# Performance work log

Hardware: AMD Instinct MI355X
Metric: run time of the kernel (lower is better)

## Reference

```python
import jax, jax.numpy as jnp
import numpy as np

N_GAUSSIANS = 512
N_PIXELS = 262144  # 512x512 image


def setup_inputs() -> dict:
    key = jax.random.key(0)
    k1, k2, k3, k4, k5 = jax.random.split(key, 5)
    x = jax.random.uniform(k1, (N_PIXELS, 2), dtype=jnp.float32)
    alphas = (1.0 / N_GAUSSIANS) ** 0.5 * jax.random.uniform(k2, (N_GAUSSIANS, 1), dtype=jnp.float32)
    means = jax.random.uniform(k3, (N_GAUSSIANS, 2), dtype=jnp.float32)
    rotations = jnp.pi * jax.random.uniform(k4, (N_GAUSSIANS, 1), dtype=jnp.float32)
    scales = 0.1 * jax.random.uniform(k5, (N_GAUSSIANS, 2), dtype=jnp.float32)
    return {"x": x, "alphas": alphas, "means": means, "rotations": rotations, "scales": scales}


def _inv2x2(m):
    # m: [N, 2, 2] -> elementwise 2x2 inverse
    a, b = m[:, 0, 0], m[:, 0, 1]
    c, d = m[:, 1, 0], m[:, 1, 1]
    det = a * d - b * c
    inv = jnp.stack([jnp.stack([d, -b], axis=-1),
                     jnp.stack([-c, a], axis=-1)], axis=-2)
    return inv / det[:, None, None]


def reference(x, alphas, means, rotations, scales):
    rot = rotations[:, 0]                       # [N]
    cth, sth = jnp.cos(rot), jnp.sin(rot)
    s0, s1 = scales[:, 0], scales[:, 1]
    # RS = R @ diag(s): [N, 2, 2]
    RS = jnp.stack([s0 * cth, -s1 * sth, s0 * sth, s1 * cth], axis=-1).reshape(-1, 2, 2)
    RSSR = jnp.einsum('nij,nkj->nik', RS, RS)   # RS @ RS^T
    cov = _inv2x2(RSSR)                          # [N, 2, 2]
    rel = x[:, None, :] - means[None, :, :]      # [P, N, 2]
    q = jnp.einsum('pni,nij,pnj->pn', rel, cov, rel)  # quadratic form [P, N]
    g = jnp.exp(-q / 2)                          # [P, N]
    return g @ alphas                            # [P, 1]
```

## Files before the change

kernel.cpp:

```cpp
#include <hip/hip_runtime.h>

#define NG 512
#define NPX 262144
#define BLOCK 256
#define GTILE 4
#define PPT 4
#define GSPLIT 8
#define GPB (NG / GSPLIT)
#define QPX (NPX / PPT)

#if __has_builtin(__builtin_amdgcn_exp2f)
  #define KSCALE 0.72134752044448170368f
  #define EXPNEG(w) __builtin_amdgcn_exp2f(-(w))
#else
  #define KSCALE 0.5f
  #define EXPNEG(w) __expf(-(w))
#endif

__global__ void gsplat_prep(const float* __restrict__ alphas,
                            const float* __restrict__ means,
                            const float* __restrict__ rotations,
                            const float* __restrict__ scales,
                            float4* __restrict__ ga,
                            float2* __restrict__ gb,
                            float* __restrict__ out)
{
    int gid = blockIdx.x * blockDim.x + threadIdx.x;
    float4 z4 = make_float4(0.f, 0.f, 0.f, 0.f);
    float4* out4 = (float4*)out;
    out4[2 * gid + 0] = z4;
    out4[2 * gid + 1] = z4;
    if (gid >= NG) return;
    int n = gid;

    float rot = rotations[n];
    float sth, cth;
    sincosf(rot, &sth, &cth);
    float s0 = scales[2 * n + 0];
    float s1 = scales[2 * n + 1];
    float r00 = s0 * cth, r01 = -s1 * sth;
    float r10 = s0 * sth, r11 =  s1 * cth;
    float Ar = r00 * r00 + r01 * r01;
    float Br = r00 * r10 + r01 * r11;
    float Dr = r10 * r10 + r11 * r11;
    float det = Ar * Dr - Br * Br;
    float kc00 =  KSCALE * Dr / det;
    float kc01 = -KSCALE * Br / det;
    float p00 = sqrtf(kc00);
    float p01 = kc01 / p00;
    float p11 = sqrtf(KSCALE / Dr);
    float mx = means[2 * n + 0];
    float my = means[2 * n + 1];
    float nuoff = -(p00 * mx + p01 * my);
    float nvoff = -(p11 * my);

    ga[n] = make_float4(p00, p01, nuoff, alphas[n]);
    gb[n] = make_float2(p11, nvoff);
}

__global__ __launch_bounds__(BLOCK, 8)
void gsplat_main(const float* __restrict__ x,
                 const float4* __restrict__ ga,
                 const float2* __restrict__ gb,
                 float* __restrict__ out)
{
    int bid = blockIdx.x;
    int pixblk = bid >> 3;
    int gbase  = (bid & 7) * GPB;

    int tid = pixblk * BLOCK + threadIdx.x;
    float xx[PPT], yy[PPT];
    #pragma unroll
    for (int p = 0; p < PPT; ++p) {
        float2 pv = ((const float2*)x)[tid + p * QPX];
        xx[p] = pv.x; yy[p] = pv.y;
    }

    float acc0[PPT], acc1[PPT];
    #pragma unroll
    for (int p = 0; p < PPT; ++p) { acc0[p] = 0.0f; acc1[p] = 0.0f; }

    float4 ca[GTILE]; float2 cb[GTILE];
    float4 na[GTILE]; float2 nb[GTILE];

    #pragma unroll
    for (int j = 0; j < GTILE; ++j) { ca[j] = ga[gbase + j]; cb[j] = gb[gbase + j]; }

    #define COMPUTE_TILE(A, B)                                                \
        _Pragma("unroll")                                                     \
        for (int j = 0; j < GTILE; ++j) {                                     \
            float czu = A[j].z;              \
            float czv = B[j].y;                                               \
            _Pragma("unroll")                                                 \
            for (int p = 0; p < PPT; ++p) {                                   \
                float u = fmaf(A[j].x, xx[p], fmaf(A[j].y, yy[p], czu));      \
                float v = fmaf(B[j].x, yy[p], czv);                           \
                float w = fmaf(v, v, u * u);                                  \
                float e = EXPNEG(w);                                          \
                if (j & 1) acc1[p] = fmaf(A[j].w, e, acc1[p]);                \
                else       acc0[p] = fmaf(A[j].w, e, acc0[p]);                \
            }                                                                 \
        }

    for (int t = 0; t < GPB; t += 2 * GTILE) {
        #pragma unroll
        for (int j = 0; j < GTILE; ++j) {
            int n = gbase + ((t + GTILE + j) & (GPB - 1));
            na[j] = ga[n]; nb[j] = gb[n];
        }
        COMPUTE_TILE(ca, cb)

        #pragma unroll
        for (int j = 0; j < GTILE; ++j) {
            int n = gbase + ((t + 2 * GTILE + j) & (GPB - 1));
            ca[j] = ga[n]; cb[j] = gb[n];
        }
        COMPUTE_TILE(na, nb)
    }
    #undef COMPUTE_TILE

    #pragma unroll
    for (int p = 0; p < PPT; ++p)
        atomicAdd(&out[tid + p * QPX], acc0[p] + acc1[p]);
}

extern "C" void kernel_launch(void* const* d_in, const int* in_sizes, int n_in,
                              void* d_out, int out_size, void* d_ws, size_t ws_size,
                              hipStream_t stream) {
    const float* x         = (const float*)d_in[0];
    const float* alphas    = (const float*)d_in[1];
    const float* means     = (const float*)d_in[2];
    const float* rotations = (const float*)d_in[3];
    const float* scales    = (const float*)d_in[4];
    float* out = (float*)d_out;

    float4* ga = (float4*)d_ws;
    float2* gb = (float2*)((char*)d_ws + NG * 16);

    gsplat_prep<<<NPX / (BLOCK * 8), BLOCK, 0, stream>>>(alphas, means, rotations, scales, ga, gb, out);

    int grid = (NPX / (BLOCK * PPT)) * GSPLIT;
    gsplat_main<<<grid, BLOCK, 0, stream>>>(x, ga, gb, out);
}
```

Baseline: 94.31 us.

## Use packed 2-wide FMA vectors for pixel pairs and reduce gaussian split

Rewrites the inner loop to handle two pixels per thread with ext_vector_type float2 and elementwise fma, so the compiler can emit packed FP32 FMA instructions (v_pk_fma_f32) and halve the FMA instruction count. Pixels per thread drop from 4 to 2 and the gaussian split from 8 to 4, which keeps the same grid size with longer per-block gaussian loops and fewer atomics per output. The exp2 work is unchanged. Each gaussian load is now amortised over fewer pixels, and the packed ops may need extra moves to splat the scalar coefficients.

```diff
diff --git a/kernel.cpp b/kernel.cpp
--- a/kernel.cpp
+++ b/kernel.cpp
@@ -4,10 +4,10 @@
 #define NPX 262144
 #define BLOCK 256
 #define GTILE 4
-#define PPT 4
-#define GSPLIT 8
+#define PPT 2
+#define GSPLIT 4
 #define GPB (NG / GSPLIT)
-#define QPX (NPX / PPT)
+#define HALFPX (NPX / 2)
 
 #if __has_builtin(__builtin_amdgcn_exp2f)
   #define KSCALE 0.72134752044448170368f
@@ -16,6 +16,18 @@
   #define KSCALE 0.5f
   #define EXPNEG(w) __expf(-(w))
 #endif
+
+typedef float v2f __attribute__((ext_vector_type(2)));
+
+#if __has_builtin(__builtin_elementwise_fma)
+  #define FMA2(a, b, c) __builtin_elementwise_fma((a), (b), (c))
+#else
+  static __device__ __forceinline__ v2f FMA2(v2f a, v2f b, v2f c) {
+      v2f r; r.x = fmaf(a.x, b.x, c.x); r.y = fmaf(a.y, b.y, c.y); return r;
+  }
+#endif
+
+static __device__ __forceinline__ v2f splat2(float s) { v2f r; r.x = s; r.y = s; return r; }
 
 __global__ void gsplat_prep(const float* __restrict__ alphas,
                             const float* __restrict__ means,
@@ -65,20 +77,17 @@
                  float* __restrict__ out)
 {
     int bid = blockIdx.x;
-    int pixblk = bid >> 3;
-    int gbase  = (bid & 7) * GPB;
+    int pixblk = bid >> 2;
+    int gbase  = (bid & 3) * GPB;
 
     int tid = pixblk * BLOCK + threadIdx.x;
-    float xx[PPT], yy[PPT];
-    #pragma unroll
-    for (int p = 0; p < PPT; ++p) {
-        float2 pv = ((const float2*)x)[tid + p * QPX];
-        xx[p] = pv.x; yy[p] = pv.y;
-    }
+    float2 pv0 = ((const float2*)x)[tid];
+    float2 pv1 = ((const float2*)x)[tid + HALFPX];
+    v2f x2; x2.x = pv0.x; x2.y = pv1.x;
+    v2f y2; y2.x = pv0.y; y2.y = pv1.y;
 
-    float acc0[PPT], acc1[PPT];
-    #pragma unroll
-    for (int p = 0; p < PPT; ++p) { acc0[p] = 0.0f; acc1[p] = 0.0f; }
+    v2f accE = splat2(0.0f);
+    v2f accO = splat2(0.0f);
 
     float4 ca[GTILE]; float2 cb[GTILE];
     float4 na[GTILE]; float2 nb[GTILE];
@@ -89,17 +98,13 @@
     #define COMPUTE_TILE(A, B)                                                \
         _Pragma("unroll")                                                     \
         for (int j = 0; j < GTILE; ++j) {                                     \
-            float czu = A[j].z;              \
-            float czv = B[j].y;                                               \
-            _Pragma("unroll")                                                 \
-            for (int p = 0; p < PPT; ++p) {                                   \
-                float u = fmaf(A[j].x, xx[p], fmaf(A[j].y, yy[p], czu));      \
-                float v = fmaf(B[j].x, yy[p], czv);                           \
-                float w = fmaf(v, v, u * u);                                  \
-                float e = EXPNEG(w);                                          \
-                if (j & 1) acc1[p] = fmaf(A[j].w, e, acc1[p]);                \
-                else       acc0[p] = fmaf(A[j].w, e, acc0[p]);                \
-            }                                                                 \
+            v2f u = FMA2(splat2(A[j].x), x2,                                  \
+                         FMA2(splat2(A[j].y), y2, splat2(A[j].z)));           \
+            v2f v = FMA2(splat2(B[j].x), y2, splat2(B[j].y));                 \
+            v2f w = FMA2(v, v, u * u);                                        \
+            v2f e; e.x = EXPNEG(w.x); e.y = EXPNEG(w.y);                      \
+            if (j & 1) accO = FMA2(splat2(A[j].w), e, accO);                  \
+            else       accE = FMA2(splat2(A[j].w), e, accE);                  \
         }
 
     for (int t = 0; t < GPB; t += 2 * GTILE) {
@@ -119,9 +124,9 @@
     }
     #undef COMPUTE_TILE
 
-    #pragma unroll
-    for (int p = 0; p < PPT; ++p)
-        atomicAdd(&out[tid + p * QPX], acc0[p] + acc1[p]);
+    v2f r = accE + accO;
+    atomicAdd(&out[tid],          r.x);
+    atomicAdd(&out[tid + HALFPX], r.y);
 }
 
 extern "C" void kernel_launch(void* const* d_in, const int* in_sizes, int n_in,
```

Result: slower. 114.1 us (+21.0%).
